# Performance work log

Hardware: AMD Instinct MI355X
Metric: run time of the kernel (lower is better)

Reference implementation:

```python
import jax, jax.numpy as jnp
import numpy as np

D_MODEL = 512
N_HEADS = 8
D_K = D_MODEL // N_HEADS
LN_EPS = 1e-5


def setup_inputs() -> dict:
    key = jax.random.key(0)
    ks = jax.random.split(key, 12)
    B, S = 2, 2048
    sc = 1.0 / np.sqrt(D_MODEL)
    inp = {
        'q': jax.random.normal(ks[0], (B, S, D_MODEL), jnp.float32),
        'k': jax.random.normal(ks[1], (B, S, D_MODEL), jnp.float32),
        'v': jax.random.normal(ks[2], (B, S, D_MODEL), jnp.float32),
        'Wq': jax.random.normal(ks[3], (D_MODEL, D_MODEL), jnp.float32) * sc,
        'bq': jnp.zeros((D_MODEL,), jnp.float32),
        'Wk': jax.random.normal(ks[4], (D_MODEL, D_MODEL), jnp.float32) * sc,
        'bk': jnp.zeros((D_MODEL,), jnp.float32),
        'Wv': jax.random.normal(ks[5], (D_MODEL, D_MODEL), jnp.float32) * sc,
        'bv': jnp.zeros((D_MODEL,), jnp.float32),
        'Wo': jax.random.normal(ks[6], (D_MODEL, D_MODEL), jnp.float32) * sc,
        'bo': jnp.zeros((D_MODEL,), jnp.float32),
        'gamma': jnp.ones((D_MODEL,), jnp.float32),
        'beta': jnp.zeros((D_MODEL,), jnp.float32),
    }
    return inp


def _split_heads(x):
    B, S, _ = x.shape
    return x.reshape(B, S, N_HEADS, D_K).transpose(0, 2, 1, 3)  # [B,H,S,d_k]


def reference(q, k, v, Wq, bq, Wk, bk, Wv, bv, Wo, bo, gamma, beta):
    B, S, _ = q.shape
    Q = _split_heads(q @ Wq.T + bq)
    K = _split_heads(k @ Wk.T + bk)
    V = _split_heads(v @ Wv.T + bv)
    scores = jnp.einsum('bhqd,bhkd->bhqk', Q, K) / jnp.sqrt(jnp.float32(D_K))
    attn = jax.nn.softmax(scores, axis=-1)  # [B,H,S,S]
    out = jnp.einsum('bhqk,bhkd->bhqd', attn, V)
    out = out.transpose(0, 2, 1, 3).reshape(B, S, D_MODEL)
    out = out @ Wo.T + bo
    x = out + q  # residual
    mu = jnp.mean(x, axis=-1, keepdims=True)
    var = jnp.mean(jnp.square(x - mu), axis=-1, keepdims=True)
    y = (x - mu) * jax.lax.rsqrt(var + LN_EPS) * gamma + beta
    return (y, attn)
```

## Files before the change

kernel.cpp:

```cpp
#include <hip/hip_runtime.h>
#include <hip/hip_bf16.h>

typedef __attribute__((ext_vector_type(8))) short short8;
typedef __attribute__((ext_vector_type(4))) short short4v;
typedef __attribute__((ext_vector_type(4))) float f32x4;

#define MFMA16(A, B, C) __builtin_amdgcn_mfma_f32_16x16x32_bf16(A, B, C, 0, 0, 0)

#define SEQ 2048
#define DM 512
#define NH 8
#define DK 64
#define NROWS 4096
#define NSPLIT 2
#define KBS (SEQ / NSPLIT)

__device__ __forceinline__ short f2bf(float f) {
  union { float f; unsigned u; } x; x.f = f;
  unsigned r = (x.u + 0x7fffu + ((x.u >> 16) & 1u)) >> 16;
  return (short)r;
}
__device__ __forceinline__ float bf2f(short s) {
  union { unsigned u; float f; } x; x.u = ((unsigned)(unsigned short)s) << 16;
  return x.f;
}

__global__ __launch_bounds__(256) void qkv_proj_kernel(
    const float* __restrict__ qin, const float* __restrict__ kin, const float* __restrict__ vin,
    const float* __restrict__ Wq, const float* __restrict__ Wk, const float* __restrict__ Wv,
    const float* __restrict__ bq, const float* __restrict__ bk, const float* __restrict__ bv,
    short* __restrict__ Qb, short* __restrict__ Kb, short* __restrict__ Vtb)
{
  int z = blockIdx.z;
  const float* X    = (z == 0) ? qin : (z == 1) ? kin : vin;
  const float* W    = (z == 0) ? Wq  : (z == 1) ? Wk  : Wv;
  const float* bias = (z == 0) ? bq  : (z == 1) ? bk  : bv;

  __shared__ short As[64][40];
  __shared__ short Bs[64][40];

  int t = threadIdx.x;
  int lane = t & 63, wave = t >> 6;
  int wr = wave >> 1, wc = wave & 1;
  int fr = lane & 15, fg = lane >> 4;
  int m0 = blockIdx.x * 64, n0 = blockIdx.y * 64;
  int lrow = t >> 2, lcol = (t & 3) * 8;

  f32x4 acc[2][2] = {};

  for (int k0 = 0; k0 < DM; k0 += 32) {
    __syncthreads();
    {
      const float* ap = X + (size_t)(m0 + lrow) * DM + k0 + lcol;
      float4 f0 = *(const float4*)ap;
      float4 f1 = *(const float4*)(ap + 4);
      short8 s;
      s[0] = f2bf(f0.x); s[1] = f2bf(f0.y); s[2] = f2bf(f0.z); s[3] = f2bf(f0.w);
      s[4] = f2bf(f1.x); s[5] = f2bf(f1.y); s[6] = f2bf(f1.z); s[7] = f2bf(f1.w);
      *(short8*)&As[lrow][lcol] = s;
      const float* bp = W + (size_t)(n0 + lrow) * DM + k0 + lcol;
      float4 g0 = *(const float4*)bp;
      float4 g1 = *(const float4*)(bp + 4);
      short8 sb;
      sb[0] = f2bf(g0.x); sb[1] = f2bf(g0.y); sb[2] = f2bf(g0.z); sb[3] = f2bf(g0.w);
      sb[4] = f2bf(g1.x); sb[5] = f2bf(g1.y); sb[6] = f2bf(g1.z); sb[7] = f2bf(g1.w);
      *(short8*)&Bs[lrow][lcol] = sb;
    }
    __syncthreads();
    short8 a0 = *(const short8*)&As[wr * 32 + fr][fg * 8];
    short8 a1 = *(const short8*)&As[wr * 32 + 16 + fr][fg * 8];
    short8 b0 = *(const short8*)&Bs[wc * 32 + fr][fg * 8];
    short8 b1 = *(const short8*)&Bs[wc * 32 + 16 + fr][fg * 8];
    acc[0][0] = MFMA16(a0, b0, acc[0][0]);
    acc[0][1] = MFMA16(a0, b1, acc[0][1]);
    acc[1][0] = MFMA16(a1, b0, acc[1][0]);
    acc[1][1] = MFMA16(a1, b1, acc[1][1]);
  }

#pragma unroll
  for (int mi = 0; mi < 2; mi++)
#pragma unroll
    for (int ni = 0; ni < 2; ni++)
#pragma unroll
      for (int r = 0; r < 4; r++) {
        int row = m0 + wr * 32 + mi * 16 + fg * 4 + r;
        int col = n0 + wc * 32 + ni * 16 + fr;
        float val = acc[mi][ni][r] + bias[col];
        int bb = row >> 11, s = row & 2047, h = col >> 6, dk = col & 63;
        short o = f2bf(val);
        if (z == 0)      Qb[((size_t)(bb * NH + h) * SEQ + s) * DK + dk] = o;
        else if (z == 1) Kb[((size_t)(bb * NH + h) * SEQ + s) * DK + dk] = o;
        else             Vtb[((size_t)(bb * NH + h) * DK + dk) * SEQ + s] = o;
      }
}

__global__ __launch_bounds__(256) void den_kernel(
    const short* __restrict__ Q, const short* __restrict__ K, float* __restrict__ dp)
{
  __shared__ short Ks[64][72];

  int t = threadIdx.x, lane = t & 63, wave = t >> 6;
  int fr = lane & 15, fg = lane >> 4;
  int bh = blockIdx.y, z = blockIdx.z;
  const short* Qh = Q + (size_t)bh * SEQ * DK;
  const short* Kh = K + (size_t)bh * SEQ * DK;
  int q0 = blockIdx.x * 64 + wave * 16;

  short8 qa0 = *(const short8*)(Qh + (q0 + fr) * DK + fg * 8);
  short8 qa1 = *(const short8*)(Qh + (q0 + fr) * DK + 32 + fg * 8);

  int r_st = t >> 2, c_st = (t & 3) * 16;

  float esum[4] = {0.f, 0.f, 0.f, 0.f};

  for (int kt = 0; kt < KBS / 64; kt++) {
    int kb = z * KBS + kt * 64;
    __syncthreads();
    {
      const short* kp = Kh + (size_t)(kb + r_st) * DK + c_st;
      *(short8*)&Ks[r_st][c_st]     = *(const short8*)kp;
      *(short8*)&Ks[r_st][c_st + 8] = *(const short8*)(kp + 8);
    }
    __syncthreads();
#pragma unroll
    for (int ct = 0; ct < 4; ct++) {
      short8 k0v = *(const short8*)&Ks[ct * 16 + fr][fg * 8];
      short8 k1v = *(const short8*)&Ks[ct * 16 + fr][32 + fg * 8];
      f32x4 zz = {0.f, 0.f, 0.f, 0.f};
      zz = MFMA16(qa0, k0v, zz);
      zz = MFMA16(qa1, k1v, zz);
#pragma unroll
      for (int r = 0; r < 4; r++)
        esum[r] += __expf(zz[r] * 0.125f);
    }
  }

#pragma unroll
  for (int r = 0; r < 4; r++) {
    float e = esum[r];
    e += __shfl_xor(e, 1);
    e += __shfl_xor(e, 2);
    e += __shfl_xor(e, 4);
    e += __shfl_xor(e, 8);
    if (fr == 0)
      dp[((size_t)z * 16 + bh) * SEQ + q0 + fg * 4 + r] = e;
  }
}

__global__ __launch_bounds__(256) void attn_pv_kernel(
    const short* __restrict__ Q, const short* __restrict__ K, const short* __restrict__ Vt,
    const float* __restrict__ dp, float* __restrict__ attn, short* __restrict__ ctxp)
{
  __shared__ short Ks[64][72];
  __shared__ short Vs[64][72];
  __shared__ short P[4][16][72];

  int t = threadIdx.x, lane = t & 63, wave = t >> 6;
  int fr = lane & 15, fg = lane >> 4;
  int bh = blockIdx.y, z = blockIdx.z;
  const short* Qh = Q + (size_t)bh * SEQ * DK;
  const short* Kh = K + (size_t)bh * SEQ * DK;
  const short* Vh = Vt + (size_t)bh * DK * SEQ;
  int q0 = blockIdx.x * 64 + wave * 16;

  short8 qa0 = *(const short8*)(Qh + (q0 + fr) * DK + fg * 8);
  short8 qa1 = *(const short8*)(Qh + (q0 + fr) * DK + 32 + fg * 8);

  float rden[4];
#pragma unroll
  for (int r = 0; r < 4; r++) {
    int row = q0 + fg * 4 + r;
    float d = dp[((size_t)0 * 16 + bh) * SEQ + row] + dp[((size_t)1 * 16 + bh) * SEQ + row];
    rden[r] = 1.f / d;
  }

  int r_st = t >> 2, c_st = (t & 3) * 16;
  int rlo = lane >> 4, c4 = (lane & 15) * 4;

  f32x4 oacc[4] = {};

  for (int kt = 0; kt < KBS / 64; kt++) {
    int kb = z * KBS + kt * 64;
    __syncthreads();
    {
      const short* kp = Kh + (size_t)(kb + r_st) * DK + c_st;
      *(short8*)&Ks[r_st][c_st]     = *(const short8*)kp;
      *(short8*)&Ks[r_st][c_st + 8] = *(const short8*)(kp + 8);
      const short* vp = Vh + (size_t)r_st * SEQ + kb + c_st;
      *(short8*)&Vs[r_st][c_st]     = *(const short8*)vp;
      *(short8*)&Vs[r_st][c_st + 8] = *(const short8*)(vp + 8);
    }
    __syncthreads();

    f32x4 sc[4];
#pragma unroll
    for (int ct = 0; ct < 4; ct++) {
      short8 k0v = *(const short8*)&Ks[ct * 16 + fr][fg * 8];
      short8 k1v = *(const short8*)&Ks[ct * 16 + fr][32 + fg * 8];
      f32x4 zz = {0.f, 0.f, 0.f, 0.f};
      zz = MFMA16(qa0, k0v, zz);
      zz = MFMA16(qa1, k1v, zz);
      sc[ct] = zz;
    }

#pragma unroll
    for (int ct = 0; ct < 4; ct++)
#pragma unroll
      for (int r = 0; r < 4; r++) {
        float p = __expf(sc[ct][r] * 0.125f) * rden[r];
        P[wave][fg * 4 + r][ct * 16 + fr] = f2bf(p);
      }
    asm volatile("s_waitcnt lgkmcnt(0)" ::: "memory");

#pragma unroll
    for (int jr = 0; jr < 4; jr++) {
      int row = jr * 4 + rlo;
      short4v pv4 = *(const short4v*)&P[wave][row][c4];
      f32x4 vv = {bf2f(pv4[0]), bf2f(pv4[1]), bf2f(pv4[2]), bf2f(pv4[3])};
      __builtin_nontemporal_store(vv,
          (f32x4*)&attn[((size_t)(bh * SEQ + q0 + row)) * SEQ + kb + c4]);
    }

    short8 pa0 = *(const short8*)&P[wave][fr][fg * 8];
    short8 pa1 = *(const short8*)&P[wave][fr][32 + fg * 8];
#pragma unroll
    for (int dt = 0; dt < 4; dt++) {
      short8 v0 = *(const short8*)&Vs[dt * 16 + fr][fg * 8];
      short8 v1 = *(const short8*)&Vs[dt * 16 + fr][32 + fg * 8];
      oacc[dt] = MFMA16(pa0, v0, oacc[dt]);
      oacc[dt] = MFMA16(pa1, v1, oacc[dt]);
    }
  }

  int b = bh >> 3, h = bh & 7;
#pragma unroll
  for (int dt = 0; dt < 4; dt++)
#pragma unroll
    for (int r = 0; r < 4; r++) {
      int row = q0 + fg * 4 + r;
      ctxp[((size_t)z * NROWS + (size_t)b * SEQ + row) * DM + h * 64 + dt * 16 + fr] =
          f2bf(oacc[dt][r]);
    }
}

__global__ __launch_bounds__(256) void oproj_kernel(
    const short* __restrict__ ctxp, const float* __restrict__ W,
    const float* __restrict__ bias, const float* __restrict__ resid,
    float* __restrict__ xout)
{
  const size_t NPART = (size_t)NROWS * DM;
  __shared__ short As[64][40];
  __shared__ short Bs[64][40];

  int t = threadIdx.x;
  int lane = t & 63, wave = t >> 6;
  int wr = wave >> 1, wc = wave & 1;
  int fr = lane & 15, fg = lane >> 4;
  int m0 = blockIdx.x * 64, n0 = blockIdx.y * 64;
  int lrow = t >> 2, lcol = (t & 3) * 8;

  f32x4 acc[2][2] = {};

  for (int k0 = 0; k0 < DM; k0 += 32) {
    __syncthreads();
    {
      size_t i = (size_t)(m0 + lrow) * DM + k0 + lcol;
      short8 sv0 = *(const short8*)(ctxp + i);
      short8 sv1 = *(const short8*)(ctxp + NPART + i);
      short8 sv;
#pragma unroll
      for (int j = 0; j < 8; j++)
        sv[j] = f2bf(bf2f(sv0[j]) + bf2f(sv1[j]));
      *(short8*)&As[lrow][lcol] = sv;
      const float* bp = W + (size_t)(n0 + lrow) * DM + k0 + lcol;
      float4 g0 = *(const float4*)bp;
      float4 g1 = *(const float4*)(bp + 4);
      short8 sb;
      sb[0] = f2bf(g0.x); sb[1] = f2bf(g0.y); sb[2] = f2bf(g0.z); sb[3] = f2bf(g0.w);
      sb[4] = f2bf(g1.x); sb[5] = f2bf(g1.y); sb[6] = f2bf(g1.z); sb[7] = f2bf(g1.w);
      *(short8*)&Bs[lrow][lcol] = sb;
    }
    __syncthreads();
    short8 a0 = *(const short8*)&As[wr * 32 + fr][fg * 8];
    short8 a1 = *(const short8*)&As[wr * 32 + 16 + fr][fg * 8];
    short8 b0 = *(const short8*)&Bs[wc * 32 + fr][fg * 8];
    short8 b1 = *(const short8*)&Bs[wc * 32 + 16 + fr][fg * 8];
    acc[0][0] = MFMA16(a0, b0, acc[0][0]);
    acc[0][1] = MFMA16(a0, b1, acc[0][1]);
    acc[1][0] = MFMA16(a1, b0, acc[1][0]);
    acc[1][1] = MFMA16(a1, b1, acc[1][1]);
  }

#pragma unroll
  for (int mi = 0; mi < 2; mi++)
#pragma unroll
    for (int ni = 0; ni < 2; ni++)
#pragma unroll
      for (int r = 0; r < 4; r++) {
        int row = m0 + wr * 32 + mi * 16 + fg * 4 + r;
        int col = n0 + wc * 32 + ni * 16 + fr;
        float val = acc[mi][ni][r] + bias[col] + resid[(size_t)row * DM + col];
        xout[(size_t)row * DM + col] = val;
      }
}

__global__ __launch_bounds__(256) void ln_kernel(
    const float* __restrict__ x, const float* __restrict__ gamma,
    const float* __restrict__ beta, float* __restrict__ y)
{
  int row = blockIdx.x * 4 + (threadIdx.x >> 6);
  int lane = threadIdx.x & 63;
  const float4* xr = (const float4*)(x + (size_t)row * DM);
  float4 v0 = xr[lane * 2];
  float4 v1 = xr[lane * 2 + 1];
  float s = v0.x + v0.y + v0.z + v0.w + v1.x + v1.y + v1.z + v1.w;
#pragma unroll
  for (int off = 1; off < 64; off <<= 1) s += __shfl_xor(s, off);
  float mean = s * (1.0f / DM);
  float a0 = v0.x - mean, a1 = v0.y - mean, a2 = v0.z - mean, a3 = v0.w - mean;
  float a4 = v1.x - mean, a5 = v1.y - mean, a6 = v1.z - mean, a7 = v1.w - mean;
  float vs = a0 * a0 + a1 * a1 + a2 * a2 + a3 * a3 + a4 * a4 + a5 * a5 + a6 * a6 + a7 * a7;
#pragma unroll
  for (int off = 1; off < 64; off <<= 1) vs += __shfl_xor(vs, off);
  float rstd = rsqrtf(vs * (1.0f / DM) + 1e-5f);
  const float4* gp = (const float4*)gamma;
  const float4* bp = (const float4*)beta;
  float4 g0 = gp[lane * 2], g1 = gp[lane * 2 + 1];
  float4 b0 = bp[lane * 2], b1 = bp[lane * 2 + 1];
  float4 o0, o1;
  o0.x = a0 * rstd * g0.x + b0.x; o0.y = a1 * rstd * g0.y + b0.y;
  o0.z = a2 * rstd * g0.z + b0.z; o0.w = a3 * rstd * g0.w + b0.w;
  o1.x = a4 * rstd * g1.x + b1.x; o1.y = a5 * rstd * g1.y + b1.y;
  o1.z = a6 * rstd * g1.z + b1.z; o1.w = a7 * rstd * g1.w + b1.w;
  float4* yr = (float4*)(y + (size_t)row * DM);
  yr[lane * 2] = o0;
  yr[lane * 2 + 1] = o1;
}

extern "C" void kernel_launch(void* const* d_in, const int* in_sizes, int n_in,
                              void* d_out, int out_size, void* d_ws, size_t ws_size,
                              hipStream_t stream)
{
  const float* q     = (const float*)d_in[0];
  const float* k     = (const float*)d_in[1];
  const float* v     = (const float*)d_in[2];
  const float* Wq    = (const float*)d_in[3];
  const float* bq    = (const float*)d_in[4];
  const float* Wk    = (const float*)d_in[5];
  const float* bk    = (const float*)d_in[6];
  const float* Wv    = (const float*)d_in[7];
  const float* bv    = (const float*)d_in[8];
  const float* Wo    = (const float*)d_in[9];
  const float* bo    = (const float*)d_in[10];
  const float* gamma = (const float*)d_in[11];
  const float* beta  = (const float*)d_in[12];

  char* w = (char*)d_ws;
  short* Qb    = (short*)(w);
  short* Kb    = (short*)(w + ((size_t)4 << 20));
  short* Vtb   = (short*)(w + ((size_t)8 << 20));
  float* denp  = (float*)(w + ((size_t)16 << 20));
  short* ctxp  = (short*)(w + ((size_t)17 << 20));
  float* xbuf  = (float*)(w + ((size_t)25 << 20));

  float* y = (float*)d_out;
  float* attnp = y + (size_t)NROWS * DM;

  qkv_proj_kernel<<<dim3(64, 8, 3), 256, 0, stream>>>(q, k, v, Wq, Wk, Wv, bq, bk, bv, Qb, Kb, Vtb);
  den_kernel<<<dim3(32, 16, NSPLIT), 256, 0, stream>>>(Qb, Kb, denp);
  attn_pv_kernel<<<dim3(32, 16, NSPLIT), 256, 0, stream>>>(Qb, Kb, Vtb, denp, attnp, ctxp);
  oproj_kernel<<<dim3(64, 8), 256, 0, stream>>>(ctxp, Wo, bo, q, xbuf);
  ln_kernel<<<1024, 256, 0, stream>>>(xbuf, gamma, beta, y);
}
```

Baseline: 146.0 us.

## Pre-cast inputs and weights to bf16 and register-prefetch tiles in all GEMM loops

```diff
diff --git a/kernel.cpp b/kernel.cpp
--- a/kernel.cpp
+++ b/kernel.cpp
@@ -14,6 +14,7 @@
 #define NROWS 4096
 #define NSPLIT 2
 #define KBS (SEQ / NSPLIT)
+#define NT (KBS / 64)
 
 __device__ __forceinline__ short f2bf(float f) {
   union { float f; unsigned u; } x; x.f = f;
@@ -25,15 +26,49 @@
   return x.f;
 }
 
+__global__ __launch_bounds__(256) void cast3_kernel(
+    const float* __restrict__ a, const float* __restrict__ b, const float* __restrict__ c,
+    short* __restrict__ ab, short* __restrict__ bb, short* __restrict__ cb)
+{
+  int z = blockIdx.z;
+  const float* src = (z == 0) ? a : (z == 1) ? b : c;
+  short* dst = (z == 0) ? ab : (z == 1) ? bb : cb;
+  size_t i = ((size_t)blockIdx.x * 256 + threadIdx.x) * 8;
+  float4 f0 = *(const float4*)(src + i);
+  float4 f1 = *(const float4*)(src + i + 4);
+  short8 s;
+  s[0] = f2bf(f0.x); s[1] = f2bf(f0.y); s[2] = f2bf(f0.z); s[3] = f2bf(f0.w);
+  s[4] = f2bf(f1.x); s[5] = f2bf(f1.y); s[6] = f2bf(f1.z); s[7] = f2bf(f1.w);
+  *(short8*)(dst + i) = s;
+}
+
+__global__ __launch_bounds__(256) void cast4_kernel(
+    const float* __restrict__ a, const float* __restrict__ b,
+    const float* __restrict__ c, const float* __restrict__ d,
+    short* __restrict__ ab, short* __restrict__ bb,
+    short* __restrict__ cb, short* __restrict__ db)
+{
+  int z = blockIdx.z;
+  const float* src = (z == 0) ? a : (z == 1) ? b : (z == 2) ? c : d;
+  short* dst = (z == 0) ? ab : (z == 1) ? bb : (z == 2) ? cb : db;
+  size_t i = ((size_t)blockIdx.x * 256 + threadIdx.x) * 8;
+  float4 f0 = *(const float4*)(src + i);
+  float4 f1 = *(const float4*)(src + i + 4);
+  short8 s;
+  s[0] = f2bf(f0.x); s[1] = f2bf(f0.y); s[2] = f2bf(f0.z); s[3] = f2bf(f0.w);
+  s[4] = f2bf(f1.x); s[5] = f2bf(f1.y); s[6] = f2bf(f1.z); s[7] = f2bf(f1.w);
+  *(short8*)(dst + i) = s;
+}
+
 __global__ __launch_bounds__(256) void qkv_proj_kernel(
-    const float* __restrict__ qin, const float* __restrict__ kin, const float* __restrict__ vin,
-    const float* __restrict__ Wq, const float* __restrict__ Wk, const float* __restrict__ Wv,
+    const short* __restrict__ qbf, const short* __restrict__ kbf, const short* __restrict__ vbf,
+    const short* __restrict__ Wqb, const short* __restrict__ Wkb, const short* __restrict__ Wvb,
     const float* __restrict__ bq, const float* __restrict__ bk, const float* __restrict__ bv,
     short* __restrict__ Qb, short* __restrict__ Kb, short* __restrict__ Vtb)
 {
   int z = blockIdx.z;
-  const float* X    = (z == 0) ? qin : (z == 1) ? kin : vin;
-  const float* W    = (z == 0) ? Wq  : (z == 1) ? Wk  : Wv;
+  const short* X    = (z == 0) ? qbf : (z == 1) ? kbf : vbf;
+  const short* W    = (z == 0) ? Wqb : (z == 1) ? Wkb : Wvb;
   const float* bias = (z == 0) ? bq  : (z == 1) ? bk  : bv;
 
   __shared__ short As[64][40];
@@ -48,25 +83,18 @@
 
   f32x4 acc[2][2] = {};
 
+  short8 a_pf = *(const short8*)(X + (size_t)(m0 + lrow) * DM + lcol);
+  short8 b_pf = *(const short8*)(W + (size_t)(n0 + lrow) * DM + lcol);
+
   for (int k0 = 0; k0 < DM; k0 += 32) {
     __syncthreads();
-    {
-      const float* ap = X + (size_t)(m0 + lrow) * DM + k0 + lcol;
-      float4 f0 = *(const float4*)ap;
-      float4 f1 = *(const float4*)(ap + 4);
-      short8 s;
-      s[0] = f2bf(f0.x); s[1] = f2bf(f0.y); s[2] = f2bf(f0.z); s[3] = f2bf(f0.w);
-      s[4] = f2bf(f1.x); s[5] = f2bf(f1.y); s[6] = f2bf(f1.z); s[7] = f2bf(f1.w);
-      *(short8*)&As[lrow][lcol] = s;
-      const float* bp = W + (size_t)(n0 + lrow) * DM + k0 + lcol;
-      float4 g0 = *(const float4*)bp;
-      float4 g1 = *(const float4*)(bp + 4);
-      short8 sb;
-      sb[0] = f2bf(g0.x); sb[1] = f2bf(g0.y); sb[2] = f2bf(g0.z); sb[3] = f2bf(g0.w);
-      sb[4] = f2bf(g1.x); sb[5] = f2bf(g1.y); sb[6] = f2bf(g1.z); sb[7] = f2bf(g1.w);
-      *(short8*)&Bs[lrow][lcol] = sb;
-    }
-    __syncthreads();
+    *(short8*)&As[lrow][lcol] = a_pf;
+    *(short8*)&Bs[lrow][lcol] = b_pf;
+    __syncthreads();
+    if (k0 + 32 < DM) {
+      a_pf = *(const short8*)(X + (size_t)(m0 + lrow) * DM + k0 + 32 + lcol);
+      b_pf = *(const short8*)(W + (size_t)(n0 + lrow) * DM + k0 + 32 + lcol);
+    }
     short8 a0 = *(const short8*)&As[wr * 32 + fr][fg * 8];
     short8 a1 = *(const short8*)&As[wr * 32 + 16 + fr][fg * 8];
     short8 b0 = *(const short8*)&Bs[wc * 32 + fr][fg * 8];
@@ -111,17 +139,22 @@
 
   int r_st = t >> 2, c_st = (t & 3) * 16;
 
+  const short* kp0 = Kh + (size_t)(z * KBS + r_st) * DK + c_st;
+  short8 k_pf0 = *(const short8*)kp0;
+  short8 k_pf1 = *(const short8*)(kp0 + 8);
+
   float esum[4] = {0.f, 0.f, 0.f, 0.f};
 
-  for (int kt = 0; kt < KBS / 64; kt++) {
-    int kb = z * KBS + kt * 64;
-    __syncthreads();
-    {
-      const short* kp = Kh + (size_t)(kb + r_st) * DK + c_st;
-      *(short8*)&Ks[r_st][c_st]     = *(const short8*)kp;
-      *(short8*)&Ks[r_st][c_st + 8] = *(const short8*)(kp + 8);
-    }
-    __syncthreads();
+  for (int kt = 0; kt < NT; kt++) {
+    __syncthreads();
+    *(short8*)&Ks[r_st][c_st]     = k_pf0;
+    *(short8*)&Ks[r_st][c_st + 8] = k_pf1;
+    __syncthreads();
+    if (kt + 1 < NT) {
+      const short* kp = Kh + (size_t)(z * KBS + (kt + 1) * 64 + r_st) * DK + c_st;
+      k_pf0 = *(const short8*)kp;
+      k_pf1 = *(const short8*)(kp + 8);
+    }
 #pragma unroll
     for (int ct = 0; ct < 4; ct++) {
       short8 k0v = *(const short8*)&Ks[ct * 16 + fr][fg * 8];
@@ -179,18 +212,29 @@
 
   f32x4 oacc[4] = {};
 
-  for (int kt = 0; kt < KBS / 64; kt++) {
+  const short* kp0 = Kh + (size_t)(z * KBS + r_st) * DK + c_st;
+  const short* vp0 = Vh + (size_t)r_st * SEQ + z * KBS + c_st;
+  short8 k_pf0 = *(const short8*)kp0;
+  short8 k_pf1 = *(const short8*)(kp0 + 8);
+  short8 v_pf0 = *(const short8*)vp0;
+  short8 v_pf1 = *(const short8*)(vp0 + 8);
+
+  for (int kt = 0; kt < NT; kt++) {
     int kb = z * KBS + kt * 64;
     __syncthreads();
-    {
-      const short* kp = Kh + (size_t)(kb + r_st) * DK + c_st;
-      *(short8*)&Ks[r_st][c_st]     = *(const short8*)kp;
-      *(short8*)&Ks[r_st][c_st + 8] = *(const short8*)(kp + 8);
-      const short* vp = Vh + (size_t)r_st * SEQ + kb + c_st;
-      *(short8*)&Vs[r_st][c_st]     = *(const short8*)vp;
-      *(short8*)&Vs[r_st][c_st + 8] = *(const short8*)(vp + 8);
-    }
-    __syncthreads();
+    *(short8*)&Ks[r_st][c_st]     = k_pf0;
+    *(short8*)&Ks[r_st][c_st + 8] = k_pf1;
+    *(short8*)&Vs[r_st][c_st]     = v_pf0;
+    *(short8*)&Vs[r_st][c_st + 8] = v_pf1;
+    __syncthreads();
+    if (kt + 1 < NT) {
+      const short* kp = Kh + (size_t)(kb + 64 + r_st) * DK + c_st;
+      const short* vp = Vh + (size_t)r_st * SEQ + kb + 64 + c_st;
+      k_pf0 = *(const short8*)kp;
+      k_pf1 = *(const short8*)(kp + 8);
+      v_pf0 = *(const short8*)vp;
+      v_pf1 = *(const short8*)(vp + 8);
+    }
 
     f32x4 sc[4];
 #pragma unroll
@@ -244,7 +288,7 @@
 }
 
 __global__ __launch_bounds__(256) void oproj_kernel(
-    const short* __restrict__ ctxp, const float* __restrict__ W,
+    const short* __restrict__ ctxp, const short* __restrict__ Wob,
     const float* __restrict__ bias, const float* __restrict__ resid,
     float* __restrict__ xout)
 {
@@ -261,26 +305,28 @@
 
   f32x4 acc[2][2] = {};
 
+  size_t ia0 = (size_t)(m0 + lrow) * DM + lcol;
+  short8 a_pf0 = *(const short8*)(ctxp + ia0);
+  short8 a_pf1 = *(const short8*)(ctxp + NPART + ia0);
+  short8 b_pf = *(const short8*)(Wob + (size_t)(n0 + lrow) * DM + lcol);
+
   for (int k0 = 0; k0 < DM; k0 += 32) {
     __syncthreads();
     {
-      size_t i = (size_t)(m0 + lrow) * DM + k0 + lcol;
-      short8 sv0 = *(const short8*)(ctxp + i);
-      short8 sv1 = *(const short8*)(ctxp + NPART + i);
       short8 sv;
 #pragma unroll
       for (int j = 0; j < 8; j++)
-        sv[j] = f2bf(bf2f(sv0[j]) + bf2f(sv1[j]));
+        sv[j] = f2bf(bf2f(a_pf0[j]) + bf2f(a_pf1[j]));
       *(short8*)&As[lrow][lcol] = sv;
-      const float* bp = W + (size_t)(n0 + lrow) * DM + k0 + lcol;
-      float4 g0 = *(const float4*)bp;
-      float4 g1 = *(const float4*)(bp + 4);
-      short8 sb;
-      sb[0] = f2bf(g0.x); sb[1] = f2bf(g0.y); sb[2] = f2bf(g0.z); sb[3] = f2bf(g0.w);
-      sb[4] = f2bf(g1.x); sb[5] = f2bf(g1.y); sb[6] = f2bf(g1.z); sb[7] = f2bf(g1.w);
-      *(short8*)&Bs[lrow][lcol] = sb;
-    }
-    __syncthreads();
+      *(short8*)&Bs[lrow][lcol] = b_pf;
+    }
+    __syncthreads();
+    if (k0 + 32 < DM) {
+      size_t ia = (size_t)(m0 + lrow) * DM + k0 + 32 + lcol;
+      a_pf0 = *(const short8*)(ctxp + ia);
+      a_pf1 = *(const short8*)(ctxp + NPART + ia);
+      b_pf = *(const short8*)(Wob + (size_t)(n0 + lrow) * DM + k0 + 32 + lcol);
+    }
     short8 a0 = *(const short8*)&As[wr * 32 + fr][fg * 8];
     short8 a1 = *(const short8*)&As[wr * 32 + 16 + fr][fg * 8];
     short8 b0 = *(const short8*)&Bs[wc * 32 + fr][fg * 8];
@@ -356,19 +402,29 @@
   const float* beta  = (const float*)d_in[12];
 
   char* w = (char*)d_ws;
-  short* Qb    = (short*)(w);
-  short* Kb    = (short*)(w + ((size_t)4 << 20));
-  short* Vtb   = (short*)(w + ((size_t)8 << 20));
-  float* denp  = (float*)(w + ((size_t)16 << 20));
-  short* ctxp  = (short*)(w + ((size_t)17 << 20));
-  float* xbuf  = (float*)(w + ((size_t)25 << 20));
+  short* qbf  = (short*)(w);
+  short* kbf  = (short*)(w + ((size_t)4  << 20));
+  short* vbf  = (short*)(w + ((size_t)8  << 20));
+  short* Qb   = (short*)(w + ((size_t)12 << 20));
+  short* Kb   = (short*)(w + ((size_t)16 << 20));
+  short* Vtb  = (short*)(w + ((size_t)20 << 20));
+  short* Wqb  = (short*)(w + ((size_t)24 << 20));
+  short* Wkb  = (short*)(w + ((size_t)24 << 20) + ((size_t)512 << 10));
+  short* Wvb  = (short*)(w + ((size_t)25 << 20));
+  short* Wob  = (short*)(w + ((size_t)25 << 20) + ((size_t)512 << 10));
+  float* denp = (float*)(w + ((size_t)26 << 20));
+  short* ctxp = (short*)(w);
+  float* xbuf = (float*)(w + ((size_t)8 << 20));
 
   float* y = (float*)d_out;
   float* attnp = y + (size_t)NROWS * DM;
 
-  qkv_proj_kernel<<<dim3(64, 8, 3), 256, 0, stream>>>(q, k, v, Wq, Wk, Wv, bq, bk, bv, Qb, Kb, Vtb);
+  cast3_kernel<<<dim3(1024, 1, 3), 256, 0, stream>>>(q, k, v, qbf, kbf, vbf);
+  cast4_kernel<<<dim3(128, 1, 4), 256, 0, stream>>>(Wq, Wk, Wv, Wo, Wqb, Wkb, Wvb, Wob);
+  qkv_proj_kernel<<<dim3(64, 8, 3), 256, 0, stream>>>(qbf, kbf, vbf, Wqb, Wkb, Wvb,
+                                                      bq, bk, bv, Qb, Kb, Vtb);
   den_kernel<<<dim3(32, 16, NSPLIT), 256, 0, stream>>>(Qb, Kb, denp);
   attn_pv_kernel<<<dim3(32, 16, NSPLIT), 256, 0, stream>>>(Qb, Kb, Vtb, denp, attnp, ctxp);
-  oproj_kernel<<<dim3(64, 8), 256, 0, stream>>>(ctxp, Wo, bo, q, xbuf);
+  oproj_kernel<<<dim3(64, 8), 256, 0, stream>>>(ctxp, Wob, bo, q, xbuf);
   ln_kernel<<<1024, 256, 0, stream>>>(xbuf, gamma, beta, y);
 }
```

Result: no change. 143.3 us (-1.9%).
